# Kernel tuning notes

Hardware: AMD Instinct MI355X
Metric: run time of the kernel (lower is better)

Reference implementation:

```python
import jax, jax.numpy as jnp
import numpy as np

NUM_EMBEDDINGS = 8192
EMBEDDING_DIM = 256
BETA = 0.25


def setup_inputs() -> dict:
    key = jax.random.key(0)
    k1, k2 = jax.random.split(key)
    z = jax.random.normal(k1, (16, 256, 32, 32), dtype=jnp.float32)
    # nn.Embedding weight init: uniform(-1/K, 1/K)
    emb = jax.random.uniform(k2, (NUM_EMBEDDINGS, EMBEDDING_DIM), dtype=jnp.float32,
                             minval=-1.0 / NUM_EMBEDDINGS, maxval=1.0 / NUM_EMBEDDINGS)
    return {"z": z, "emb": emb}


def reference(z, emb):
    b, c, h, w = z.shape
    flat = z.transpose(0, 2, 3, 1).reshape(-1, c)  # [B*H*W, C]
    distances = (jnp.sum(flat * flat, axis=1, keepdims=True)
                 - 2.0 * flat @ emb.T
                 + jnp.sum(emb * emb, axis=1))  # [B*H*W, K]
    indices = jnp.argmin(distances, axis=1)  # [B*H*W]
    quantized = emb[indices].reshape(b, h, w, c).transpose(0, 3, 1, 2)  # [B,C,H,W]
    codebook_loss = jnp.mean((jax.lax.stop_gradient(quantized) - z) ** 2)
    commitment_loss = BETA * jnp.mean((quantized - jax.lax.stop_gradient(z)) ** 2)
    quantized_st = z + jax.lax.stop_gradient(quantized - z)  # straight-through
    return quantized_st, codebook_loss, commitment_loss, indices.reshape(b, h, w)
```

## Files before the change

kernel.cpp:

```cpp
#include <hip/hip_runtime.h>

#define NROWS   16384
#define KCODES  8192
#define CDIM    256
#define HWS     1024
#define BSTRIDE 262144

#define WS_AN   0
#define WS_CE   16384
#define WS_CD   24576
#define WS_CI   155648
#define WS_IDX  286720
#define WS_LOSS 303104

typedef float f32x2 __attribute__((ext_vector_type(2)));
typedef float f32x4 __attribute__((ext_vector_type(4)));

#define PKFMA_LO(acc, a, b) \
  asm("v_pk_fma_f32 %0, %1, %2, %0 op_sel:[0,0,0] op_sel_hi:[0,1,1]" \
      : "+v"(acc) : "v"(a), "v"(b))
#define PKFMA_HI(acc, a, b) \
  asm("v_pk_fma_f32 %0, %1, %2, %0 op_sel:[1,0,0] op_sel_hi:[1,1,1]" \
      : "+v"(acc) : "v"(a), "v"(b))

__global__ void rownorm_z_k(const float* __restrict__ z, float* __restrict__ An) {
#pragma clang fp contract(off)
  int n = blockIdx.x * 256 + threadIdx.x;
  const float* base = z + ((size_t)(n >> 10)) * BSTRIDE + (n & 1023);
  float hs[2];
  for (int h = 0; h < 2; ++h) {
    float r[8];
#pragma unroll
    for (int j = 0; j < 8; ++j) { float v = base[(size_t)(h * 128 + j) * HWS]; r[j] = v * v; }
    for (int m = 1; m < 16; ++m) {
#pragma unroll
      for (int j = 0; j < 8; ++j) { float v = base[(size_t)(h * 128 + m * 8 + j) * HWS]; r[j] += v * v; }
    }
    hs[h] = ((r[0] + r[1]) + (r[2] + r[3])) + ((r[4] + r[5]) + (r[6] + r[7]));
  }
  An[n] = hs[0] + hs[1];
}

__global__ void rownorm_e_k(const float* __restrict__ emb, float* __restrict__ Ce) {
#pragma clang fp contract(off)
  int n = blockIdx.x * 256 + threadIdx.x;
  const float* base = emb + (size_t)n * CDIM;
  float hs[2];
  for (int h = 0; h < 2; ++h) {
    float r[8];
#pragma unroll
    for (int j = 0; j < 8; ++j) { float v = base[h * 128 + j]; r[j] = v * v; }
    for (int m = 1; m < 16; ++m) {
#pragma unroll
      for (int j = 0; j < 8; ++j) { float v = base[h * 128 + m * 8 + j]; r[j] += v * v; }
    }
    hs[h] = ((r[0] + r[1]) + (r[2] + r[3])) + ((r[4] + r[5]) + (r[6] + r[7]));
  }
  Ce[n] = hs[0] + hs[1];
}

__global__ void __launch_bounds__(256)
vq_argmin_k(const float* __restrict__ z, const float* __restrict__ emb,
            const float* __restrict__ An, const float* __restrict__ Ce,
            float* __restrict__ cand_d, int* __restrict__ cand_i) {
  __shared__ float smem[8192];
  float* As = smem;
  float* Bs = smem + 4096;

  const int t  = threadIdx.x;
  const int tx = t & 15;
  const int ty = t >> 4;
  const int tile  = blockIdx.x >> 3;
  const int slice = blockIdx.x & 7;
  const int rbase = tile * 128;
  const int k0    = slice * 1024;

  const float* zb = z + ((size_t)(rbase >> 10)) * BSTRIDE + (rbase & 1023);

  float best[8];
  int   bidx[8];
#pragma unroll
  for (int ri = 0; ri < 8; ++ri) { best[ri] = 3.4028235e38f; bidx[ri] = 0; }

  f32x2 acc2[8][4];
#pragma unroll
  for (int ri = 0; ri < 8; ++ri)
#pragma unroll
    for (int j = 0; j < 4; ++j) acc2[ri][j] = (f32x2){0.f, 0.f};

  const int a_c   = t >> 4;
  const int a_hw  = (t & 15) * 8;
  const int a_swr = (t & 15) & 7;
  const int a_wi  = a_c & 3;
  const int a_kg1 = a_c >> 2;
  const int acol1 = ((a_kg1 ^ a_swr) << 2) | a_wi;
  const int acol2 = (((a_kg1 + 4) ^ a_swr) << 2) | a_wi;
  const int b_code = t >> 1;
  const int b_cb   = (t & 1) * 16;
  const int b_p    = ((b_code >> 5) << 4) | (b_code & 15);
  const int b_s    = (b_code >> 4) & 1;
  const int b_p7   = b_code & 7;
  const int b_base = b_p * 64 + ((b_cb >> 1) << 2) + b_s;

  const int rd_a_sw = ty & 7;
  const int rd_b_sw = tx & 7;
  const int bB      = tx * 64;

  for (int kc = 0; kc < 8; ++kc) {
    const int kbase = k0 + kc * 128;
#pragma unroll 1
    for (int sc = 0; sc < 8; ++sc) {
      const float* zsrc = zb + (size_t)(sc * 32 + a_c) * HWS + a_hw;
      const float4 pa0 = *(const float4*)(zsrc);
      const float4 pa1 = *(const float4*)(zsrc + 4);
      const float4 pa2 = *(const float4*)(zsrc + 16 * HWS);
      const float4 pa3 = *(const float4*)(zsrc + 16 * HWS + 4);
      const float* bsrc = emb + (size_t)(kbase + b_code) * CDIM + sc * 32 + b_cb;
      const float4 pb0 = *(const float4*)(bsrc);
      const float4 pb1 = *(const float4*)(bsrc + 4);
      const float4 pb2 = *(const float4*)(bsrc + 8);
      const float4 pb3 = *(const float4*)(bsrc + 12);

      __syncthreads();
      {
        const float va0[8] = {pa0.x, pa0.y, pa0.z, pa0.w, pa1.x, pa1.y, pa1.z, pa1.w};
        const float va1[8] = {pa2.x, pa2.y, pa2.z, pa2.w, pa3.x, pa3.y, pa3.z, pa3.w};
#pragma unroll
        for (int j = 0; j < 8; ++j) {
          const int rb = (a_hw + j) << 5;
          As[rb + acol1] = va0[j];
          As[rb + acol2] = va1[j];
        }
        const float bval[16] = {pb0.x, pb0.y, pb0.z, pb0.w,
                                pb1.x, pb1.y, pb1.z, pb1.w,
                                pb2.x, pb2.y, pb2.z, pb2.w,
                                pb3.x, pb3.y, pb3.z, pb3.w};
#pragma unroll
        for (int i = 0; i < 8; ++i) {
          const int off = b_base + ((i ^ b_p7) << 2);
          Bs[off]     = bval[2 * i];
          Bs[off + 2] = bval[2 * i + 1];
        }
      }
      __syncthreads();

#pragma unroll
      for (int g = 0; g < 8; ++g) {
        const int sw0 = ((2 * g) ^ rd_b_sw) << 2;
        const int sw1 = sw0 ^ 4;
        f32x4 bv[8];
#pragma unroll
        for (int ci2 = 0; ci2 < 4; ++ci2) {
          bv[ci2 * 2 + 0] = *(const f32x4*)&Bs[bB + ci2 * 1024 + sw0];
          bv[ci2 * 2 + 1] = *(const f32x4*)&Bs[bB + ci2 * 1024 + sw1];
        }
#pragma unroll
        for (int ri = 0; ri < 8; ++ri) {
          const f32x4 a = *(const f32x4*)&As[((ty * 8 + ri) << 5) + ((g ^ rd_a_sw) << 2)];
          const f32x2 a01 = __builtin_shufflevector(a, a, 0, 1);
          const f32x2 a23 = __builtin_shufflevector(a, a, 2, 3);
#pragma unroll
          for (int ci2 = 0; ci2 < 4; ++ci2) {
            const f32x2 bk0 = __builtin_shufflevector(bv[ci2 * 2 + 0], bv[ci2 * 2 + 0], 0, 1);
            const f32x2 bk1 = __builtin_shufflevector(bv[ci2 * 2 + 0], bv[ci2 * 2 + 0], 2, 3);
            const f32x2 bk2 = __builtin_shufflevector(bv[ci2 * 2 + 1], bv[ci2 * 2 + 1], 0, 1);
            const f32x2 bk3 = __builtin_shufflevector(bv[ci2 * 2 + 1], bv[ci2 * 2 + 1], 2, 3);
            PKFMA_HI(acc2[ri][ci2], a23, bk3);
            PKFMA_LO(acc2[ri][ci2], a23, bk2);
            PKFMA_HI(acc2[ri][ci2], a01, bk1);
            PKFMA_LO(acc2[ri][ci2], a01, bk0);
          }
        }
      }
    }

    {
      const int kkb = kbase + tx;
      float cearr[8];
#pragma unroll
      for (int ci = 0; ci < 8; ++ci) cearr[ci] = Ce[kkb + ci * 16];
#pragma unroll
      for (int ri = 0; ri < 8; ++ri) {
        const float Ar = An[rbase + ty * 8 + ri];
#pragma unroll
        for (int ci2 = 0; ci2 < 4; ++ci2) {
          const float d0 = (Ar - 2.0f * acc2[ri][ci2].x) + cearr[2 * ci2];
          if (d0 < best[ri]) { best[ri] = d0; bidx[ri] = kkb + ci2 * 32; }
          const float d1 = (Ar - 2.0f * acc2[ri][ci2].y) + cearr[2 * ci2 + 1];
          if (d1 < best[ri]) { best[ri] = d1; bidx[ri] = kkb + ci2 * 32 + 16; }
          acc2[ri][ci2] = (f32x2){0.f, 0.f};
        }
      }
    }
  }

  __syncthreads();
  float* redd = smem;
  int*   redi = (int*)(smem + 2048);
#pragma unroll
  for (int ri = 0; ri < 8; ++ri) {
    redd[(ty * 8 + ri) * 16 + tx] = best[ri];
    redi[(ty * 8 + ri) * 16 + tx] = bidx[ri];
  }
  __syncthreads();
  if (t < 128) {
    float bd = redd[t * 16];
    int   bi = redi[t * 16];
    for (int j = 1; j < 16; ++j) {
      const float d  = redd[t * 16 + j];
      const int   i2 = redi[t * 16 + j];
      if (d < bd || (d == bd && i2 < bi)) { bd = d; bi = i2; }
    }
    const int n = rbase + t;
    cand_d[n * 8 + slice] = bd;
    cand_i[n * 8 + slice] = bi;
  }
}

__global__ void vq_merge_k(const float* __restrict__ cand_d, const int* __restrict__ cand_i,
                           int* __restrict__ idx_final, float* __restrict__ idxf_out) {
  const int n = blockIdx.x * 256 + threadIdx.x;
  float bd = cand_d[n * 8];
  int   bi = cand_i[n * 8];
#pragma unroll
  for (int s = 1; s < 8; ++s) {
    const float d  = cand_d[n * 8 + s];
    const int   i2 = cand_i[n * 8 + s];
    if (d < bd || (d == bd && i2 < bi)) { bd = d; bi = i2; }
  }
  idx_final[n] = bi;
  idxf_out[n] = (float)bi;
}

__launch_bounds__(256)
__global__ void vq_gather_loss_k(const float* __restrict__ z, const float* __restrict__ emb,
                                 const int* __restrict__ idx_final,
                                 float* __restrict__ qout, float* __restrict__ loss_acc) {
  __shared__ float Qs[32 * 260];
  __shared__ int   kidx[32];
  __shared__ float warp_s[4];
  const int t = threadIdx.x;
  const int rbase = blockIdx.x * 32;
  if (t < 32) kidx[t] = idx_final[rbase + t];
  __syncthreads();
  {
    const int r = t >> 3, cp = t & 7;
    const float4* er = (const float4*)(emb + (size_t)kidx[r] * CDIM);
#pragma unroll
    for (int j = 0; j < 8; ++j) {
      const int c4 = cp + j * 8;
      const float4 v = er[c4];
      *(float4*)&Qs[r * 260 + c4 * 4] = v;
    }
  }
  __syncthreads();
  const int b = rbase >> 10, hw0 = rbase & 1023;
  const float* zb = z + (size_t)b * BSTRIDE + hw0;
  float* qb = qout + (size_t)b * BSTRIDE + hw0;
  float s = 0.f;
  const int hwl = t & 31, cg = t >> 5;
  for (int i = 0; i < 32; ++i) {
    const int c = cg * 32 + i;
    const float q  = Qs[hwl * 260 + c];
    const size_t off = (size_t)c * HWS + hwl;
    const float zv = zb[off];
    const float d  = q - zv;
    qb[off] = zv + d;
    s += d * d;
  }
  for (int off = 32; off; off >>= 1) s += __shfl_down(s, off, 64);
  if ((t & 63) == 0) warp_s[t >> 6] = s;
  __syncthreads();
  if (t == 0) atomicAdd(loss_acc, warp_s[0] + warp_s[1] + warp_s[2] + warp_s[3]);
}

__global__ void vq_finalize_k(const float* __restrict__ loss_acc, float* __restrict__ out_loss) {
  const float m = loss_acc[0] * (1.0f / 4194304.0f);
  out_loss[0] = m;
  out_loss[1] = 0.25f * m;
}

extern "C" void kernel_launch(void* const* d_in, const int* in_sizes, int n_in,
                              void* d_out, int out_size, void* d_ws, size_t ws_size,
                              hipStream_t stream) {
  (void)in_sizes; (void)n_in; (void)out_size; (void)ws_size;
  const float* z   = (const float*)d_in[0];
  const float* emb = (const float*)d_in[1];
  float* out      = (float*)d_out;
  float* q_out    = out;
  float* loss_out = out + 4194304;
  float* idxf_out = out + 4194306;

  float* ws       = (float*)d_ws;
  float* An       = ws + WS_AN;
  float* Ce       = ws + WS_CE;
  float* cand_d   = ws + WS_CD;
  int*   cand_i   = (int*)(ws + WS_CI);
  int*   idx_fin  = (int*)(ws + WS_IDX);
  float* loss_acc = ws + WS_LOSS;

  hipMemsetAsync(loss_acc, 0, sizeof(float), stream);
  rownorm_z_k<<<64, 256, 0, stream>>>(z, An);
  rownorm_e_k<<<32, 256, 0, stream>>>(emb, Ce);
  vq_argmin_k<<<1024, 256, 0, stream>>>(z, emb, An, Ce, cand_d, cand_i);
  vq_merge_k<<<64, 256, 0, stream>>>(cand_d, cand_i, idx_fin, idxf_out);
  vq_gather_loss_k<<<512, 256, 0, stream>>>(z, emb, idx_fin, q_out, loss_acc);
  vq_finalize_k<<<1, 1, 0, stream>>>(loss_acc, loss_out);
}
```

Before: 990.8 us.

## Widen argmin register tile to 128x256 codes and halve codebook slices

Each block of the distance/argmin kernel now covers 256 codes per chunk instead of 128, doubling the per-thread accumulator tile to 8x16 and the shared B tile. The codebook is split into 4 slices instead of 8, halving the grid and the candidate merge work. The inner loop is reordered to hold A fragments in registers and stream B. The aim is higher arithmetic intensity and less reloading of z per code, at the cost of more register pressure and lower occupancy (launch bounds set to 2 blocks) with only 512 blocks on the device.

```diff
diff --git a/kernel.cpp b/kernel.cpp
--- a/kernel.cpp
+++ b/kernel.cpp
@@ -9,9 +9,9 @@
 #define WS_AN   0
 #define WS_CE   16384
 #define WS_CD   24576
-#define WS_CI   155648
-#define WS_IDX  286720
-#define WS_LOSS 303104
+#define WS_CI   90112
+#define WS_IDX  155648
+#define WS_LOSS 172032
 
 typedef float f32x2 __attribute__((ext_vector_type(2)));
 typedef float f32x4 __attribute__((ext_vector_type(4)));
@@ -59,21 +59,21 @@
   Ce[n] = hs[0] + hs[1];
 }
 
-__global__ void __launch_bounds__(256)
+__global__ void __launch_bounds__(256, 2)
 vq_argmin_k(const float* __restrict__ z, const float* __restrict__ emb,
             const float* __restrict__ An, const float* __restrict__ Ce,
             float* __restrict__ cand_d, int* __restrict__ cand_i) {
-  __shared__ float smem[8192];
+  __shared__ float smem[12288];
   float* As = smem;
   float* Bs = smem + 4096;
 
   const int t  = threadIdx.x;
   const int tx = t & 15;
   const int ty = t >> 4;
-  const int tile  = blockIdx.x >> 3;
-  const int slice = blockIdx.x & 7;
+  const int tile  = blockIdx.x >> 2;
+  const int slice = blockIdx.x & 3;
   const int rbase = tile * 128;
-  const int k0    = slice * 1024;
+  const int k0    = slice * 2048;
 
   const float* zb = z + ((size_t)(rbase >> 10)) * BSTRIDE + (rbase & 1023);
 
@@ -82,11 +82,11 @@
 #pragma unroll
   for (int ri = 0; ri < 8; ++ri) { best[ri] = 3.4028235e38f; bidx[ri] = 0; }
 
-  f32x2 acc2[8][4];
+  f32x2 acc2[8][8];
 #pragma unroll
   for (int ri = 0; ri < 8; ++ri)
 #pragma unroll
-    for (int j = 0; j < 4; ++j) acc2[ri][j] = (f32x2){0.f, 0.f};
+    for (int j = 0; j < 8; ++j) acc2[ri][j] = (f32x2){0.f, 0.f};
 
   const int a_c   = t >> 4;
   const int a_hw  = (t & 15) * 8;
@@ -107,7 +107,7 @@
   const int bB      = tx * 64;
 
   for (int kc = 0; kc < 8; ++kc) {
-    const int kbase = k0 + kc * 128;
+    const int kbase = k0 + kc * 256;
 #pragma unroll 1
     for (int sc = 0; sc < 8; ++sc) {
       const float* zsrc = zb + (size_t)(sc * 32 + a_c) * HWS + a_hw;
@@ -115,11 +115,16 @@
       const float4 pa1 = *(const float4*)(zsrc + 4);
       const float4 pa2 = *(const float4*)(zsrc + 16 * HWS);
       const float4 pa3 = *(const float4*)(zsrc + 16 * HWS + 4);
-      const float* bsrc = emb + (size_t)(kbase + b_code) * CDIM + sc * 32 + b_cb;
-      const float4 pb0 = *(const float4*)(bsrc);
-      const float4 pb1 = *(const float4*)(bsrc + 4);
-      const float4 pb2 = *(const float4*)(bsrc + 8);
-      const float4 pb3 = *(const float4*)(bsrc + 12);
+      const float* bsrc0 = emb + (size_t)(kbase + b_code) * CDIM + sc * 32 + b_cb;
+      const float* bsrc1 = bsrc0 + (size_t)128 * CDIM;
+      const float4 pb0 = *(const float4*)(bsrc0);
+      const float4 pb1 = *(const float4*)(bsrc0 + 4);
+      const float4 pb2 = *(const float4*)(bsrc0 + 8);
+      const float4 pb3 = *(const float4*)(bsrc0 + 12);
+      const float4 pb4 = *(const float4*)(bsrc1);
+      const float4 pb5 = *(const float4*)(bsrc1 + 4);
+      const float4 pb6 = *(const float4*)(bsrc1 + 8);
+      const float4 pb7 = *(const float4*)(bsrc1 + 12);
 
       __syncthreads();
       {
@@ -131,40 +136,45 @@
           As[rb + acol1] = va0[j];
           As[rb + acol2] = va1[j];
         }
-        const float bval[16] = {pb0.x, pb0.y, pb0.z, pb0.w,
-                                pb1.x, pb1.y, pb1.z, pb1.w,
-                                pb2.x, pb2.y, pb2.z, pb2.w,
-                                pb3.x, pb3.y, pb3.z, pb3.w};
+        const float bval0[16] = {pb0.x, pb0.y, pb0.z, pb0.w,
+                                 pb1.x, pb1.y, pb1.z, pb1.w,
+                                 pb2.x, pb2.y, pb2.z, pb2.w,
+                                 pb3.x, pb3.y, pb3.z, pb3.w};
+        const float bval1[16] = {pb4.x, pb4.y, pb4.z, pb4.w,
+                                 pb5.x, pb5.y, pb5.z, pb5.w,
+                                 pb6.x, pb6.y, pb6.z, pb6.w,
+                                 pb7.x, pb7.y, pb7.z, pb7.w};
 #pragma unroll
         for (int i = 0; i < 8; ++i) {
           const int off = b_base + ((i ^ b_p7) << 2);
-          Bs[off]     = bval[2 * i];
-          Bs[off + 2] = bval[2 * i + 1];
+          Bs[off]            = bval0[2 * i];
+          Bs[off + 2]        = bval0[2 * i + 1];
+          Bs[off + 4096]     = bval1[2 * i];
+          Bs[off + 4096 + 2] = bval1[2 * i + 1];
         }
       }
       __syncthreads();
 
 #pragma unroll
       for (int g = 0; g < 8; ++g) {
+        f32x4 av[8];
+#pragma unroll
+        for (int ri = 0; ri < 8; ++ri)
+          av[ri] = *(const f32x4*)&As[((ty * 8 + ri) << 5) + ((g ^ rd_a_sw) << 2)];
         const int sw0 = ((2 * g) ^ rd_b_sw) << 2;
         const int sw1 = sw0 ^ 4;
-        f32x4 bv[8];
-#pragma unroll
-        for (int ci2 = 0; ci2 < 4; ++ci2) {
-          bv[ci2 * 2 + 0] = *(const f32x4*)&Bs[bB + ci2 * 1024 + sw0];
-          bv[ci2 * 2 + 1] = *(const f32x4*)&Bs[bB + ci2 * 1024 + sw1];
-        }
-#pragma unroll
-        for (int ri = 0; ri < 8; ++ri) {
-          const f32x4 a = *(const f32x4*)&As[((ty * 8 + ri) << 5) + ((g ^ rd_a_sw) << 2)];
-          const f32x2 a01 = __builtin_shufflevector(a, a, 0, 1);
-          const f32x2 a23 = __builtin_shufflevector(a, a, 2, 3);
-#pragma unroll
-          for (int ci2 = 0; ci2 < 4; ++ci2) {
-            const f32x2 bk0 = __builtin_shufflevector(bv[ci2 * 2 + 0], bv[ci2 * 2 + 0], 0, 1);
-            const f32x2 bk1 = __builtin_shufflevector(bv[ci2 * 2 + 0], bv[ci2 * 2 + 0], 2, 3);
-            const f32x2 bk2 = __builtin_shufflevector(bv[ci2 * 2 + 1], bv[ci2 * 2 + 1], 0, 1);
-            const f32x2 bk3 = __builtin_shufflevector(bv[ci2 * 2 + 1], bv[ci2 * 2 + 1], 2, 3);
+#pragma unroll
+        for (int ci2 = 0; ci2 < 8; ++ci2) {
+          const f32x4 b0 = *(const f32x4*)&Bs[bB + ci2 * 1024 + sw0];
+          const f32x4 b1 = *(const f32x4*)&Bs[bB + ci2 * 1024 + sw1];
+          const f32x2 bk0 = __builtin_shufflevector(b0, b0, 0, 1);
+          const f32x2 bk1 = __builtin_shufflevector(b0, b0, 2, 3);
+          const f32x2 bk2 = __builtin_shufflevector(b1, b1, 0, 1);
+          const f32x2 bk3 = __builtin_shufflevector(b1, b1, 2, 3);
+#pragma unroll
+          for (int ri = 0; ri < 8; ++ri) {
+            const f32x2 a01 = __builtin_shufflevector(av[ri], av[ri], 0, 1);
+            const f32x2 a23 = __builtin_shufflevector(av[ri], av[ri], 2, 3);
             PKFMA_HI(acc2[ri][ci2], a23, bk3);
             PKFMA_LO(acc2[ri][ci2], a23, bk2);
             PKFMA_HI(acc2[ri][ci2], a01, bk1);
@@ -176,14 +186,14 @@
 
     {
       const int kkb = kbase + tx;
-      float cearr[8];
-#pragma unroll
-      for (int ci = 0; ci < 8; ++ci) cearr[ci] = Ce[kkb + ci * 16];
+      float cearr[16];
+#pragma unroll
+      for (int ci = 0; ci < 16; ++ci) cearr[ci] = Ce[kkb + ci * 16];
 #pragma unroll
       for (int ri = 0; ri < 8; ++ri) {
         const float Ar = An[rbase + ty * 8 + ri];
 #pragma unroll
-        for (int ci2 = 0; ci2 < 4; ++ci2) {
+        for (int ci2 = 0; ci2 < 8; ++ci2) {
           const float d0 = (Ar - 2.0f * acc2[ri][ci2].x) + cearr[2 * ci2];
           if (d0 < best[ri]) { best[ri] = d0; bidx[ri] = kkb + ci2 * 32; }
           const float d1 = (Ar - 2.0f * acc2[ri][ci2].y) + cearr[2 * ci2 + 1];
@@ -212,20 +222,20 @@
       if (d < bd || (d == bd && i2 < bi)) { bd = d; bi = i2; }
     }
     const int n = rbase + t;
-    cand_d[n * 8 + slice] = bd;
-    cand_i[n * 8 + slice] = bi;
+    cand_d[n * 4 + slice] = bd;
+    cand_i[n * 4 + slice] = bi;
   }
 }
 
 __global__ void vq_merge_k(const float* __restrict__ cand_d, const int* __restrict__ cand_i,
                            int* __restrict__ idx_final, float* __restrict__ idxf_out) {
   const int n = blockIdx.x * 256 + threadIdx.x;
-  float bd = cand_d[n * 8];
-  int   bi = cand_i[n * 8];
-#pragma unroll
-  for (int s = 1; s < 8; ++s) {
-    const float d  = cand_d[n * 8 + s];
-    const int   i2 = cand_i[n * 8 + s];
+  float bd = cand_d[n * 4];
+  int   bi = cand_i[n * 4];
+#pragma unroll
+  for (int s = 1; s < 4; ++s) {
+    const float d  = cand_d[n * 4 + s];
+    const int   i2 = cand_i[n * 4 + s];
     if (d < bd || (d == bd && i2 < bi)) { bd = d; bi = i2; }
   }
   idx_final[n] = bi;
@@ -302,7 +312,7 @@
   hipMemsetAsync(loss_acc, 0, sizeof(float), stream);
   rownorm_z_k<<<64, 256, 0, stream>>>(z, An);
   rownorm_e_k<<<32, 256, 0, stream>>>(emb, Ce);
-  vq_argmin_k<<<1024, 256, 0, stream>>>(z, emb, An, Ce, cand_d, cand_i);
+  vq_argmin_k<<<512, 256, 0, stream>>>(z, emb, An, Ce, cand_d, cand_i);
   vq_merge_k<<<64, 256, 0, stream>>>(cand_d, cand_i, idx_fin, idxf_out);
   vq_gather_loss_k<<<512, 256, 0, stream>>>(z, emb, idx_fin, q_out, loss_acc);
   vq_finalize_k<<<1, 1, 0, stream>>>(loss_acc, loss_out);
```

Result: faster. 899.0 us (-9.3%).
